# Kernel tuning notes

Hardware: AMD Instinct MI355X
Metric: run time of the kernel (lower is better)

The kernel has to match this reference:

```python
import jax, jax.numpy as jnp
import numpy as np

NEG_SLOPE = 0.01  # torch F.leaky_relu default

def setup_inputs() -> dict:
    key = jax.random.key(0)
    k1, k2, k3 = jax.random.split(key, 3)
    N, V, F_in, H = 32, 1024, 128, 64
    features = jax.random.normal(k1, (N, V, F_in), dtype=jnp.float32)
    # torch nn.Linear weights: W: [H, F_in], a: [1, 2H]
    W = jax.random.normal(k2, (H, F_in), dtype=jnp.float32) * (1.0 / np.sqrt(F_in))
    a = jax.random.normal(k3, (1, 2 * H), dtype=jnp.float32) * (1.0 / np.sqrt(2 * H))
    return {"features": features, "W": W, "a": a}

def reference(features, W, a):
    N, V, _ = features.shape
    H = W.shape[0]
    # h = features @ W^T : [N, V, H]
    h = jnp.einsum('nvf,hf->nvh', features, W)
    # The concat-linear trick decomposes: a([h_i ; h_j]) = h_i @ a_src + h_j @ a_dst
    a_src = a[0, :H]   # [H]
    a_dst = a[0, H:]   # [H]
    s_src = h @ a_src  # [N, V]  (score contribution of node i)
    s_dst = h @ a_dst  # [N, V]  (score contribution of node j)
    e = s_src[:, :, None] + s_dst[:, None, :]          # [N, V, V]
    e = jnp.where(e >= 0, e, NEG_SLOPE * e)            # leaky_relu
    attention = jax.nn.softmax(e, axis=2)              # softmax over j
    h_prime = jnp.einsum('nij,njh->nih', attention, h) # [N, V, H]
    return h_prime
```

## Files before the change

### kernel.cpp

```cpp
#include <hip/hip_runtime.h>
#include <hip/hip_bf16.h>

#define NEG_SLOPE 0.01f

constexpr int N_G  = 32;
constexpr int V_N  = 1024;
constexpr int F_IN = 128;
constexpr int H_D  = 64;
constexpr int NV   = N_G * V_N;

typedef __attribute__((ext_vector_type(8))) short bf16x8;
typedef __attribute__((ext_vector_type(4))) float f32x4;

__device__ __forceinline__ float bf16bits_to_f32(unsigned short u) {
    unsigned int x = ((unsigned int)u) << 16;
    return __builtin_bit_cast(float, x);
}
__device__ __forceinline__ unsigned short f32_to_bf16bits(float f) {
    return __builtin_bit_cast(unsigned short, __float2bfloat16(f));
}


__global__ __launch_bounds__(256) void gat_h_mfma(
    const float* __restrict__ feat,
    const float* __restrict__ W,
    const float* __restrict__ a,
    __hip_bfloat16* __restrict__ hT,
    float* __restrict__ s_src,
    float* __restrict__ s_dst)
{
    __shared__ __align__(16) float Fs[64][132];
    __shared__ __align__(16) unsigned short Wf[16384];

    const int tid  = threadIdx.x;
    const int lane = tid & 63;
    const int w    = tid >> 6;
    const int mb   = lane & 15;
    const int kg   = lane >> 4;
    const int r0   = blockIdx.x * 64;

#pragma unroll
    for (int t = 0; t < 8; ++t) {
        int f4  = tid + t * 256;
        int row = f4 >> 5;
        int c4  = (f4 & 31) << 2;
        float4 v = *reinterpret_cast<const float4*>(
            feat + (size_t)(r0 + row) * F_IN + c4);
        *reinterpret_cast<float4*>(&Fs[row][c4]) = v;
    }
#pragma unroll
    for (int t = 0; t < 8; ++t) {
        int f4 = tid + t * 256;
        int n  = f4 >> 5;
        int k4 = (f4 & 31) << 2;
        float4 v = *reinterpret_cast<const float4*>(W + (size_t)n * F_IN + k4);
        int ks  = k4 >> 5;
        int kgw = (k4 >> 3) & 3;
        int rr  = k4 & 7;
        int tt  = n >> 4, nn = n & 15;
        float fv[4] = {v.x, v.y, v.z, v.w};
        unsigned long long ph = 0, pl = 0;
#pragma unroll
        for (int e = 0; e < 4; ++e) {
            unsigned short hb = f32_to_bf16bits(fv[e]);
            unsigned short lb = f32_to_bf16bits(fv[e] - bf16bits_to_f32(hb));
            ph |= ((unsigned long long)hb) << (16 * e);
            pl |= ((unsigned long long)lb) << (16 * e);
        }
        char* base = (char*)Wf;
        int chunk  = (ks * 4 + tt) * 2;
        int off    = (kgw * 16 + nn) * 16 + rr * 2;
        *reinterpret_cast<unsigned long long*>(base + chunk * 1024 + off)       = ph;
        *reinterpret_cast<unsigned long long*>(base + (chunk + 1) * 1024 + off) = pl;
    }
    __syncthreads();

    f32x4 acc[4];
#pragma unroll
    for (int t = 0; t < 4; ++t) acc[t] = (f32x4){0.f, 0.f, 0.f, 0.f};

    const char* wfb = (const char*)Wf;
#pragma unroll
    for (int ks = 0; ks < 4; ++ks) {
        float af[8];
        *reinterpret_cast<float4*>(&af[0]) =
            *reinterpret_cast<const float4*>(&Fs[w * 16 + mb][ks * 32 + kg * 8]);
        *reinterpret_cast<float4*>(&af[4]) =
            *reinterpret_cast<const float4*>(&Fs[w * 16 + mb][ks * 32 + kg * 8 + 4]);
        bf16x8 Ah, Al;
#pragma unroll
        for (int e = 0; e < 8; ++e) {
            unsigned short hb = f32_to_bf16bits(af[e]);
            Ah[e] = (short)hb;
            Al[e] = (short)f32_to_bf16bits(af[e] - bf16bits_to_f32(hb));
        }
#pragma unroll
        for (int t = 0; t < 4; ++t) {
            bf16x8 Bh = *reinterpret_cast<const bf16x8*>(
                wfb + (size_t)((ks * 4 + t) * 2) * 1024 + lane * 16);
            bf16x8 Bl = *reinterpret_cast<const bf16x8*>(
                wfb + (size_t)((ks * 4 + t) * 2 + 1) * 1024 + lane * 16);
            acc[t] = __builtin_amdgcn_mfma_f32_16x16x32_bf16(Al, Bh, acc[t], 0, 0, 0);
            acc[t] = __builtin_amdgcn_mfma_f32_16x16x32_bf16(Ah, Bl, acc[t], 0, 0, 0);
            acc[t] = __builtin_amdgcn_mfma_f32_16x16x32_bf16(Ah, Bh, acc[t], 0, 0, 0);
        }
    }

    float asrc[4], adst[4];
#pragma unroll
    for (int t = 0; t < 4; ++t) {
        asrc[t] = a[t * 16 + mb];
        adst[t] = a[H_D + t * 16 + mb];
    }
    float ps[4], pd[4];
#pragma unroll
    for (int reg = 0; reg < 4; ++reg) {
        ps[reg] = acc[0][reg] * asrc[0] + acc[1][reg] * asrc[1]
                + acc[2][reg] * asrc[2] + acc[3][reg] * asrc[3];
        pd[reg] = acc[0][reg] * adst[0] + acc[1][reg] * adst[1]
                + acc[2][reg] * adst[2] + acc[3][reg] * adst[3];
    }
#pragma unroll
    for (int off = 1; off < 16; off <<= 1) {
#pragma unroll
        for (int reg = 0; reg < 4; ++reg) {
            ps[reg] += __shfl_xor(ps[reg], off);
            pd[reg] += __shfl_xor(pd[reg], off);
        }
    }
    if (mb == 0) {
#pragma unroll
        for (int reg = 0; reg < 4; ++reg) {
            int j = w * 16 + kg * 4 + reg;
            s_src[r0 + j] = ps[reg];
            s_dst[r0 + j] = pd[reg];
        }
    }

    __syncthreads();
    float (*FsT)[65] = reinterpret_cast<float(*)[65]>(&Fs[0][0]);
#pragma unroll
    for (int t = 0; t < 4; ++t)
#pragma unroll
        for (int reg = 0; reg < 4; ++reg)
            FsT[w * 16 + kg * 4 + reg][t * 16 + mb] = acc[t][reg];
    __syncthreads();

    const int g  = r0 >> 10;
    const int jt = (r0 & (V_N - 1)) >> 6;
    char* tile = (char*)(hT + (size_t)g * H_D * V_N) + (size_t)jt * 8192;
#pragma unroll
    for (int ch = 0; ch < 2; ++ch) {
        int chi = tid * 2 + ch;
        int tp  = chi >> 7;
        int kk  = (chi >> 6) & 1;
        int kgp = (chi >> 4) & 3;
        int mp  = chi & 15;
        int c   = tp * 16 + mp;
        int jb  = kk * 32 + kgp * 8;
        unsigned short outp[8];
#pragma unroll
        for (int rr = 0; rr < 8; ++rr) outp[rr] = f32_to_bf16bits(FsT[jb + rr][c]);
        *reinterpret_cast<int4*>(tile + (size_t)chi * 16) =
            *reinterpret_cast<const int4*>(outp);
    }
}

__global__ __launch_bounds__(256) void gat_attn_mfma(
    const __hip_bfloat16* __restrict__ hT,
    const float* __restrict__ s_src,
    const float* __restrict__ s_dst,
    float* __restrict__ out)
{
    __shared__ float sd[V_N];
    __shared__ float wred[4];
    __shared__ int4 hbuf[2][512];

    const int tid  = threadIdx.x;
    const int lane = tid & 63;
    const int wv   = tid >> 6;
    const int m    = lane & 15;
    const int kg   = lane >> 4;
    const int n    = blockIdx.x >> 4;
    const int i0   = (blockIdx.x & 15) * 64;
    const size_t nbase = (size_t)n * V_N;

    const char* hTg = (const char*)(hT + (size_t)n * H_D * V_N);

    float lm;
    {
        float4 v = *reinterpret_cast<const float4*>(s_dst + nbase + tid * 4);
        *reinterpret_cast<float4*>(&sd[tid * 4]) = v;
        lm = fmaxf(fmaxf(v.x, v.y), fmaxf(v.z, v.w));
    }
#pragma unroll
    for (int off = 32; off >= 1; off >>= 1)
        lm = fmaxf(lm, __shfl_xor(lm, off));
    if (lane == 0) wred[wv] = lm;

    const int row  = i0 + wv * 16 + m;
    const float ss = s_src[nbase + row];

    {
        int4 s0 = *reinterpret_cast<const int4*>(hTg + tid * 32);
        int4 s1 = *reinterpret_cast<const int4*>(hTg + tid * 32 + 16);
        hbuf[0][tid * 2]     = s0;
        hbuf[0][tid * 2 + 1] = s1;
    }
    __syncthreads();

    const float M    = fmaxf(fmaxf(wred[0], wred[1]), fmaxf(wred[2], wred[3]));
    const float t0   = ss + M;
    const float negm = -fmaxf(t0, NEG_SLOPE * t0);

    f32x4 accC[4];
    f32x4 accD = {0.f, 0.f, 0.f, 0.f};
#pragma unroll
    for (int t = 0; t < 4; ++t) accC[t] = (f32x4){0.f, 0.f, 0.f, 0.f};

    bf16x8 ones;
#pragma unroll
    for (int r = 0; r < 8; ++r) ones[r] = (short)0x3F80;

    int cur = 0;
    for (int jt = 0; jt < V_N / 64; ++jt) {
        int4 n0, n1;
        if (jt < V_N / 64 - 1) {
            const char* g = hTg + (size_t)(jt + 1) * 8192 + tid * 32;
            n0 = *reinterpret_cast<const int4*>(g);
            n1 = *reinterpret_cast<const int4*>(g + 16);
        }

        const char* bb = (const char*)&hbuf[cur][0];
#pragma unroll
        for (int kk = 0; kk < 2; ++kk) {
            float p[8];
            *reinterpret_cast<float4*>(&p[0]) =
                *reinterpret_cast<const float4*>(&sd[jt * 64 + kk * 32 + kg * 8]);
            *reinterpret_cast<float4*>(&p[4]) =
                *reinterpret_cast<const float4*>(&sd[jt * 64 + kk * 32 + kg * 8 + 4]);

            bf16x8 A;
#pragma unroll
            for (int r = 0; r < 8; ++r) {
                float tt = ss + p[r];
                float l  = fmaxf(tt, NEG_SLOPE * tt);
                float w  = __expf(l + negm);
                A[r] = (short)__builtin_bit_cast(unsigned short, __float2bfloat16(w));
            }

            accD = __builtin_amdgcn_mfma_f32_16x16x32_bf16(A, ones, accD, 0, 0, 0);
#pragma unroll
            for (int t = 0; t < 4; ++t) {
                bf16x8 B = *reinterpret_cast<const bf16x8*>(
                    bb + (t * 2 + kk) * 1024 + lane * 16);
                accC[t] = __builtin_amdgcn_mfma_f32_16x16x32_bf16(A, B, accC[t], 0, 0, 0);
            }
        }

        if (jt < V_N / 64 - 1) {
            hbuf[cur ^ 1][tid * 2]     = n0;
            hbuf[cur ^ 1][tid * 2 + 1] = n1;
        }
        __syncthreads();
        cur ^= 1;
    }

    float inv[4];
#pragma unroll
    for (int r = 0; r < 4; ++r) inv[r] = 1.0f / accD[r];
#pragma unroll
    for (int r = 0; r < 4; ++r) {
        const size_t ob = (nbase + i0 + wv * 16 + kg * 4 + r) * H_D;
#pragma unroll
        for (int t = 0; t < 4; ++t)
            out[ob + t * 16 + m] = accC[t][r] * inv[r];
    }
}

extern "C" void kernel_launch(void* const* d_in, const int* in_sizes, int n_in,
                              void* d_out, int out_size, void* d_ws, size_t ws_size,
                              hipStream_t stream) {
    const float* feat = (const float*)d_in[0];
    const float* W    = (const float*)d_in[1];
    const float* a    = (const float*)d_in[2];
    float* out = (float*)d_out;

    __hip_bfloat16* hT = (__hip_bfloat16*)d_ws;
    float* s_src = (float*)(hT + (size_t)NV * H_D);
    float* s_dst = s_src + NV;

    gat_h_mfma<<<NV / 64, 256, 0, stream>>>(feat, W, a, hT, s_src, s_dst);
    gat_attn_mfma<<<N_G * (V_N / 64), 256, 0, stream>>>(hT, s_src, s_dst, out);
}
```

Baseline: 89.74 us.

## Split attention j-loop across wave pairs and halve rows per block

Each attention block now covers 32 rows instead of 64, and the grid doubles to 1024 blocks. Within a block, two waves cover each 16-row group and split the j-range between them, each taking alternate 64-column tiles from a double-buffered shared tile of 128 columns. Partial numerators and denominators from the second half are combined through shared memory before normalisation. This aims to raise parallelism and occupancy, at the cost of loading every h tile twice as often across blocks plus an extra reduction step.

```diff
diff --git a/kernel.cpp b/kernel.cpp
--- a/kernel.cpp
+++ b/kernel.cpp
@@ -174,15 +174,17 @@
 {
     __shared__ float sd[V_N];
     __shared__ float wred[4];
-    __shared__ int4 hbuf[2][512];
-
-    const int tid  = threadIdx.x;
-    const int lane = tid & 63;
-    const int wv   = tid >> 6;
-    const int m    = lane & 15;
-    const int kg   = lane >> 4;
-    const int n    = blockIdx.x >> 4;
-    const int i0   = (blockIdx.x & 15) * 64;
+    __shared__ __align__(16) int4 hbuf[2][2][512];
+
+    const int tid   = threadIdx.x;
+    const int lane  = tid & 63;
+    const int wv    = tid >> 6;
+    const int rowhalf = wv & 1;
+    const int jhalf   = wv >> 1;
+    const int m     = lane & 15;
+    const int kg    = lane >> 4;
+    const int n     = blockIdx.x >> 5;
+    const int i0    = (blockIdx.x & 31) * 32;
     const size_t nbase = (size_t)n * V_N;
 
     const char* hTg = (const char*)(hT + (size_t)n * H_D * V_N);
@@ -198,14 +200,13 @@
         lm = fmaxf(lm, __shfl_xor(lm, off));
     if (lane == 0) wred[wv] = lm;
 
-    const int row  = i0 + wv * 16 + m;
-    const float ss = s_src[nbase + row];
-
-    {
-        int4 s0 = *reinterpret_cast<const int4*>(hTg + tid * 32);
-        int4 s1 = *reinterpret_cast<const int4*>(hTg + tid * 32 + 16);
-        hbuf[0][tid * 2]     = s0;
-        hbuf[0][tid * 2 + 1] = s1;
+    const float ss = s_src[nbase + i0 + rowhalf * 16 + m];
+
+#pragma unroll
+    for (int par = 0; par < 2; ++par) {
+        const char* g = hTg + (size_t)par * 8192 + tid * 32;
+        hbuf[0][par][tid * 2]     = *reinterpret_cast<const int4*>(g);
+        hbuf[0][par][tid * 2 + 1] = *reinterpret_cast<const int4*>(g + 16);
     }
     __syncthreads();
 
@@ -222,16 +223,19 @@
 #pragma unroll
     for (int r = 0; r < 8; ++r) ones[r] = (short)0x3F80;
 
-    int cur = 0;
-    for (int jt = 0; jt < V_N / 64; ++jt) {
-        int4 n0, n1;
-        if (jt < V_N / 64 - 1) {
-            const char* g = hTg + (size_t)(jt + 1) * 8192 + tid * 32;
-            n0 = *reinterpret_cast<const int4*>(g);
-            n1 = *reinterpret_cast<const int4*>(g + 16);
-        }
-
-        const char* bb = (const char*)&hbuf[cur][0];
+    for (int s = 0; s < 8; ++s) {
+        int4 n00, n01, n10, n11;
+        if (s < 7) {
+            const char* g0 = hTg + (size_t)(2 * s + 2) * 8192 + tid * 32;
+            const char* g1 = hTg + (size_t)(2 * s + 3) * 8192 + tid * 32;
+            n00 = *reinterpret_cast<const int4*>(g0);
+            n01 = *reinterpret_cast<const int4*>(g0 + 16);
+            n10 = *reinterpret_cast<const int4*>(g1);
+            n11 = *reinterpret_cast<const int4*>(g1 + 16);
+        }
+
+        const int jt   = 2 * s + jhalf;
+        const char* bb = (const char*)&hbuf[s & 1][jhalf][0];
 #pragma unroll
         for (int kk = 0; kk < 2; ++kk) {
             float p[8];
@@ -258,23 +262,39 @@
             }
         }
 
-        if (jt < V_N / 64 - 1) {
-            hbuf[cur ^ 1][tid * 2]     = n0;
-            hbuf[cur ^ 1][tid * 2 + 1] = n1;
+        if (s < 7) {
+            hbuf[(s + 1) & 1][0][tid * 2]     = n00;
+            hbuf[(s + 1) & 1][0][tid * 2 + 1] = n01;
+            hbuf[(s + 1) & 1][1][tid * 2]     = n10;
+            hbuf[(s + 1) & 1][1][tid * 2 + 1] = n11;
         }
         __syncthreads();
-        cur ^= 1;
-    }
-
-    float inv[4];
-#pragma unroll
-    for (int r = 0; r < 4; ++r) inv[r] = 1.0f / accD[r];
-#pragma unroll
-    for (int r = 0; r < 4; ++r) {
-        const size_t ob = (nbase + i0 + wv * 16 + kg * 4 + r) * H_D;
-#pragma unroll
-        for (int t = 0; t < 4; ++t)
-            out[ob + t * 16 + m] = accC[t][r] * inv[r];
+    }
+
+    float* comb = (float*)&hbuf[0][0][0];
+    float* cden = comb + 2 * 16 * 68;
+    if (jhalf == 1) {
+#pragma unroll
+        for (int reg = 0; reg < 4; ++reg) {
+            int rrow = rowhalf * 16 + kg * 4 + reg;
+#pragma unroll
+            for (int t = 0; t < 4; ++t)
+                comb[rrow * 68 + t * 16 + m] = accC[t][reg];
+            if (m == 0) cden[rrow] = accD[reg];
+        }
+    }
+    __syncthreads();
+    if (jhalf == 0) {
+#pragma unroll
+        for (int reg = 0; reg < 4; ++reg) {
+            int rrow = rowhalf * 16 + kg * 4 + reg;
+            float den = accD[reg] + cden[rrow];
+            float inv = 1.0f / den;
+            const size_t ob = (nbase + i0 + rowhalf * 16 + kg * 4 + reg) * H_D;
+#pragma unroll
+            for (int t = 0; t < 4; ++t)
+                out[ob + t * 16 + m] = (accC[t][reg] + comb[rrow * 68 + t * 16 + m]) * inv;
+        }
     }
 }
 
@@ -291,5 +311,5 @@
     float* s_dst = s_src + NV;
 
     gat_h_mfma<<<NV / 64, 256, 0, stream>>>(feat, W, a, hT, s_src, s_dst);
-    gat_attn_mfma<<<N_G * (V_N / 64), 256, 0, stream>>>(hT, s_src, s_dst, out);
-}
+    gat_attn_mfma<<<N_G * (V_N / 32), 256, 0, stream>>>(hT, s_src, s_dst, out);
+}
```

Result: no change. 88.31 us (-1.6%).
